# Kernel tuning notes

Hardware: AMD Instinct MI355X
Metric: run time of the kernel (lower is better)

Reference implementation:

```python
import jax, jax.numpy as jnp
import numpy as np

B, S, HID = 2, 2048, 2048
NH, NKV, HD = 8, 1, 256
GROUPS = NH // NKV
THETA = 10000.0


def _rope_cos_sin(position_ids, dtype):
    # inv_freq: [HD/2]
    inv_freq = 1.0 / (THETA ** (jnp.arange(0, HD, 2, dtype=jnp.float32) / HD))
    # freqs: [B, S, HD/2]
    freqs = position_ids.astype(jnp.float32)[:, :, None] * inv_freq[None, None, :]
    emb = jnp.concatenate([freqs, freqs], axis=-1)  # [B, S, HD]
    return emb.astype(dtype), None  # placeholder (cos/sin computed below)


def _rotate_half(x):
    x1, x2 = jnp.split(x, 2, axis=-1)
    return jnp.concatenate([-x2, x1], axis=-1)


def setup_inputs() -> dict:
    key = jax.random.key(0)
    ks = jax.random.split(key, 6)
    hidden_states = jax.random.normal(ks[0], (B, S, HID), dtype=jnp.float32)
    # causal additive mask, broadcast over heads: [B, 1, S, S]
    causal = jnp.tril(jnp.ones((S, S), dtype=bool))
    attention_mask = jnp.where(causal, 0.0, -1e9).astype(jnp.float32)[None, None] * jnp.ones((B, 1, 1, 1), jnp.float32)
    position_ids = jnp.broadcast_to(jnp.arange(S, dtype=jnp.int64 if jax.config.jax_enable_x64 else jnp.int32), (B, S))
    sc = 1.0 / np.sqrt(HID)
    Wq = jax.random.normal(ks[1], (HID, NH * HD), dtype=jnp.float32) * sc
    Wk = jax.random.normal(ks[2], (HID, NKV * HD), dtype=jnp.float32) * sc
    Wv = jax.random.normal(ks[3], (HID, NKV * HD), dtype=jnp.float32) * sc
    Wo = jax.random.normal(ks[4], (NH * HD, HID), dtype=jnp.float32) * sc
    return {"hidden_states": hidden_states, "attention_mask": attention_mask,
            "position_ids": position_ids, "Wq": Wq, "Wk": Wk, "Wv": Wv, "Wo": Wo}


def reference(hidden_states, attention_mask, position_ids, Wq, Wk, Wv, Wo):
    b, s, _ = hidden_states.shape
    # projections -> [b, h, s, d]
    q = (hidden_states @ Wq).reshape(b, s, NH, HD).transpose(0, 2, 1, 3)
    k = (hidden_states @ Wk).reshape(b, s, NKV, HD).transpose(0, 2, 1, 3)
    v = (hidden_states @ Wv).reshape(b, s, NKV, HD).transpose(0, 2, 1, 3)

    # RoPE cos/sin: [b, s, HD]
    inv_freq = 1.0 / (THETA ** (jnp.arange(0, HD, 2, dtype=jnp.float32) / HD))
    freqs = position_ids.astype(jnp.float32)[:, :, None] * inv_freq[None, None, :]
    emb = jnp.concatenate([freqs, freqs], axis=-1)
    cos = jnp.cos(emb).astype(hidden_states.dtype)[:, None]  # [b,1,s,HD]
    sin = jnp.sin(emb).astype(hidden_states.dtype)[:, None]
    q = q * cos + _rotate_half(q) * sin
    k = k * cos + _rotate_half(k) * sin

    # GQA without materializing repeated KV: q -> [b, g, rep, s, d]
    qg = q.reshape(b, NKV, GROUPS, s, HD)
    scale = 1.0 / np.sqrt(HD)
    scores = jnp.einsum('bgrqd,bgkd->bgrqk', qg, k) * scale  # [b,g,rep,s,s]
    scores = scores + attention_mask.reshape(b, 1, 1, s, s) if attention_mask.shape[1] == 1 else scores + attention_mask.reshape(b, NKV, GROUPS, s, s)
    attn = jax.nn.softmax(scores.astype(jnp.float32), axis=-1).astype(q.dtype)
    out = jnp.einsum('bgrqk,bgkd->bgrqd', attn, v)  # [b,g,rep,s,d]
    out = out.reshape(b, NH, s, HD).transpose(0, 2, 1, 3).reshape(b, s, NH * HD)
    attn_output = out @ Wo  # [b, s, HID]
    attn_weights = attn.reshape(b, NH, s, s)
    return attn_output, attn_weights
```

## Files before the change

### kernel.cpp

```cpp
#include <hip/hip_runtime.h>
#include <hip/hip_bf16.h>
#include <cstdint>


#define BB 2
#define SS 2048
#define HIDD 2048
#define NHH 8
#define HDD 256
#define L2E 1.44269504088896340736f
#define QSCALE 0.0625f

typedef float f32x4 __attribute__((ext_vector_type(4)));
typedef short short8 __attribute__((ext_vector_type(8)));
typedef __bf16 bf16x8 __attribute__((ext_vector_type(8)));
typedef __attribute__((address_space(1))) void gvoid;
typedef __attribute__((address_space(3))) void svoid;

__device__ __forceinline__ ushort f2bf(float f){
  union { float f; uint32_t u; } v; v.f = f;
  uint32_t r = (v.u + 0x7fffu + ((v.u >> 16) & 1u)) >> 16;
  return (ushort)r;
}
__device__ __forceinline__ float bf2f(ushort u){
  union { uint32_t u; float f; } v; v.u = ((uint32_t)u) << 16;
  return v.f;
}
__device__ __forceinline__ void gld_lds16(const ushort* gp, ushort* lp){
  __builtin_amdgcn_global_load_lds((gvoid*)gp, (svoid*)lp, 16, 0, 0);
}
__device__ __forceinline__ f32x4 mfma16(short8 a, short8 b, f32x4 c){
  return __builtin_amdgcn_mfma_f32_16x16x32_bf16(
      __builtin_bit_cast(bf16x8, a), __builtin_bit_cast(bf16x8, b), c, 0, 0, 0);
}

__global__ void k_convH(const float* __restrict__ Hf, ushort* __restrict__ Hb){
  const int n4 = (BB*SS*HIDD) >> 2;
  for (int i = blockIdx.x*256 + threadIdx.x; i < n4; i += gridDim.x*256){
    float4 v = ((const float4*)Hf)[i];
    ushort4 o; o.x=f2bf(v.x); o.y=f2bf(v.y); o.z=f2bf(v.z); o.w=f2bf(v.w);
    ((ushort4*)Hb)[i] = o;
  }
}

__global__ __launch_bounds__(256) void k_transW(const float* __restrict__ W,
                                                ushort* __restrict__ Wt,
                                                int N, int rowOff){
  __shared__ float t[64][65];
  const int n0 = blockIdx.x * 64, k0 = blockIdx.y * 64;
  const int tid = threadIdx.x;
  const int r = tid >> 4, c4 = (tid & 15) << 2;
  #pragma unroll
  for (int i = 0; i < 4; ++i){
    int rr = r + i*16;
    float4 v = *(const float4*)&W[(size_t)(k0 + rr) * N + n0 + c4];
    t[rr][c4] = v.x; t[rr][c4+1] = v.y; t[rr][c4+2] = v.z; t[rr][c4+3] = v.w;
  }
  __syncthreads();
  #pragma unroll
  for (int i = 0; i < 4; ++i){
    int nn = r + i*16;
    ushort4 o;
    o.x = f2bf(t[c4  ][nn]); o.y = f2bf(t[c4+1][nn]);
    o.z = f2bf(t[c4+2][nn]); o.w = f2bf(t[c4+3][nn]);
    *(ushort4*)&Wt[(size_t)(rowOff + n0 + nn) * 2048 + k0 + c4] = o;
  }
}

__global__ void k_costab(const int* __restrict__ pos, float2* __restrict__ cs){
  int i = blockIdx.x*256 + threadIdx.x;
  int d = i & 127, bs = i >> 7;
  float p = (float)pos[bs];
  float inv = exp2f(-(float)(2*d) * (13.287712379549449f / 256.0f));
  float f = p * inv;
  cs[i] = make_float2(cosf(f), sinf(f));
}

__global__ void k_rope(ushort* __restrict__ Qr, ushort* __restrict__ Kr,
                       const float2* __restrict__ cs){
  const int NQ = BB*SS*NHH*128;
  int i = blockIdx.x*256 + threadIdx.x;
  if (i < NQ){
    int d = i & 127, h = (i >> 7) & 7, bs = i >> 10;
    ushort* p = Qr + (size_t)bs*2048 + h*256 + d;
    float2 c = cs[bs*128 + d];
    float x1 = bf2f(p[0]), x2 = bf2f(p[128]);
    p[0]   = f2bf((x1*c.x - x2*c.y) * QSCALE);
    p[128] = f2bf((x2*c.x + x1*c.y) * QSCALE);
  } else if (i < NQ + BB*SS*128){
    int j = i - NQ;
    int d = j & 127, bs = j >> 7;
    ushort* p = Kr + (size_t)bs*256 + d;
    float2 c = cs[bs*128 + d];
    float x1 = bf2f(p[0]), x2 = bf2f(p[128]);
    p[0]   = f2bf(x1*c.x - x2*c.y);
    p[128] = f2bf(x2*c.x + x1*c.y);
  }
}

__global__ __launch_bounds__(256) void k_gemm(const ushort* __restrict__ A,
                                              const ushort* __restrict__ Bt,
                                              int Ksteps, int mode,
                                              float* __restrict__ Cf,
                                              ushort* __restrict__ Qr,
                                              ushort* __restrict__ Kr,
                                              ushort* __restrict__ Vt){
  __shared__ __align__(16) ushort As[128*32];
  __shared__ __align__(16) ushort Bs[128*32];
  const int tid = threadIdx.x;
  const int l = tid & 63, w = tid >> 6;
  const int lr = l & 15, lg = l >> 4;
  const int wr = (w >> 1) * 64, wc = (w & 1) * 64;
  const int m0 = blockIdx.y * 128, n0 = blockIdx.x * 128;
  f32x4 acc[4][4] = {};
  for (int kt = 0; kt < Ksteps; ++kt){
    const int kb = kt * 32;
    #pragma unroll
    for (int t = 0; t < 2; ++t){
      int r = t*64 + (tid >> 2), g = tid & 3;
      int gl = g ^ ((r >> 1) & 3);
      gld_lds16(A  + (size_t)(m0 + r) * 2048 + kb + gl*8, As + (t*256 + (tid & ~63))*8);
      gld_lds16(Bt + (size_t)(n0 + r) * 2048 + kb + gl*8, Bs + (t*256 + (tid & ~63))*8);
    }
    __syncthreads();
    short8 af[4], bf[4];
    #pragma unroll
    for (int mi = 0; mi < 4; ++mi){
      int r = wr + mi*16 + lr;
      af[mi] = *(const short8*)&As[r*32 + ((lg ^ ((r>>1)&3)) << 3)];
    }
    #pragma unroll
    for (int ni = 0; ni < 4; ++ni){
      int r = wc + ni*16 + lr;
      bf[ni] = *(const short8*)&Bs[r*32 + ((lg ^ ((r>>1)&3)) << 3)];
    }
    #pragma unroll
    for (int mi = 0; mi < 4; ++mi)
      #pragma unroll
      for (int ni = 0; ni < 4; ++ni)
        acc[mi][ni] = mfma16(af[mi], bf[ni], acc[mi][ni]);
    __syncthreads();
  }
  #pragma unroll
  for (int mi = 0; mi < 4; ++mi){
    #pragma unroll
    for (int ni = 0; ni < 4; ++ni){
      #pragma unroll
      for (int r = 0; r < 4; ++r){
        int row = m0 + wr + mi*16 + lg*4 + r;
        int nn  = n0 + wc + ni*16 + lr;
        float v = acc[mi][ni][r];
        if (mode == 0){
          Cf[(size_t)row * 2048 + nn] = v;
        } else {
          if (nn < 2048)      Qr[(size_t)row*2048 + nn] = f2bf(v);
          else if (nn < 2304) Kr[(size_t)row*256 + (nn - 2048)] = f2bf(v);
          else { int d = nn - 2304;
                 Vt[((size_t)(row >> 11) * 256 + d) * 2048 + (row & 2047)] = f2bf(v); }
        }
      }
    }
  }
}

__global__ __launch_bounds__(256) void k_stats(const ushort* __restrict__ Qr,
                                               const ushort* __restrict__ Kr,
                                               float* __restrict__ mpart,
                                               float* __restrict__ lpart){
  __shared__ __align__(16) ushort Ks[32*256];
  const int qt = blockIdx.x, ksp = blockIdx.y, bh = blockIdx.z;
  const int b = bh >> 3, h = bh & 7;
  const int q0 = qt * 64;
  const int nkt = (q0 + 64) >> 5;
  const int per = (nkt + 3) >> 2;
  const int t0 = ksp * per;
  const int t1 = min(nkt, t0 + per);
  const int tid = threadIdx.x;
  const int l = tid & 63, w = tid >> 6;
  const int lr = l & 15, lg = l >> 4;
  short8 qf[8];
  const ushort* qbase = Qr + ((size_t)(b*SS) + q0 + w*16 + lr) * 2048 + h*256;
  #pragma unroll
  for (int dc = 0; dc < 8; ++dc) qf[dc] = *(const short8*)&qbase[dc*32 + lg*8];
  float mrun[4], lrun[4];
  #pragma unroll
  for (int r = 0; r < 4; ++r){ mrun[r] = -3e38f; lrun[r] = 0.f; }
  for (int kt = t0; kt < t1; ++kt){
    const int k0 = kt * 32;
    #pragma unroll
    for (int t = 0; t < 4; ++t){
      int idx = t*256 + tid;
      int r = idx >> 5, g = idx & 31;
      int gl = g ^ (r & 7);
      gld_lds16(Kr + ((size_t)(b*SS) + k0 + r) * 256 + gl*8, Ks + (t*256 + (tid & ~63))*8);
    }
    __syncthreads();
    f32x4 sc0 = {0.f,0.f,0.f,0.f}, sc1 = {0.f,0.f,0.f,0.f};
    const int kr0 = lr, kr1 = 16 + lr;
    #pragma unroll
    for (int dc = 0; dc < 8; ++dc){
      short8 b0 = *(const short8*)&Ks[kr0*256 + ((dc*32 + lg*8) ^ ((kr0 & 7) << 3))];
      sc0 = mfma16(qf[dc], b0, sc0);
    }
    #pragma unroll
    for (int dc = 0; dc < 8; ++dc){
      short8 b1 = *(const short8*)&Ks[kr1*256 + ((dc*32 + lg*8) ^ ((kr1 & 7) << 3))];
      sc1 = mfma16(qf[dc], b1, sc1);
    }
    __syncthreads();
    #pragma unroll
    for (int r = 0; r < 4; ++r){
      const int qq = q0 + w*16 + lg*4 + r;
      float s0 = (k0 + lr       <= qq) ? sc0[r] : -3e38f;
      float s1 = (k0 + 16 + lr  <= qq) ? sc1[r] : -3e38f;
      float mx = fmaxf(s0, s1);
      #pragma unroll
      for (int d = 1; d < 16; d <<= 1) mx = fmaxf(mx, __shfl_xor(mx, d, 64));
      float mnew = fmaxf(mrun[r], mx);
      if (mnew > -1e37f){
        float ps = exp2f((s0 - mnew) * L2E) + exp2f((s1 - mnew) * L2E);
        #pragma unroll
        for (int d = 1; d < 16; d <<= 1) ps += __shfl_xor(ps, d, 64);
        lrun[r] = lrun[r] * exp2f((mrun[r] - mnew) * L2E) + ps;
        mrun[r] = mnew;
      }
    }
  }
  if (lr == 0){
    #pragma unroll
    for (int r = 0; r < 4; ++r){
      int qq = q0 + w*16 + lg*4 + r;
      size_t sidx = (size_t)ksp * (BB*NHH*SS) + (size_t)bh * SS + qq;
      mpart[sidx] = mrun[r];
      lpart[sidx] = lrun[r];
    }
  }
}

__global__ void k_merge(const float* __restrict__ mpart, const float* __restrict__ lpart,
                        float* __restrict__ mfin, float* __restrict__ invl){
  const int N = BB*NHH*SS;
  int i = blockIdx.x * 256 + threadIdx.x;
  if (i >= N) return;
  float m = -3e38f;
  #pragma unroll
  for (int s = 0; s < 4; ++s) m = fmaxf(m, mpart[s*N + i]);
  float lsum = 0.f;
  #pragma unroll
  for (int s = 0; s < 4; ++s){
    float ls = lpart[s*N + i];
    lsum += (ls > 0.f) ? ls * exp2f((mpart[s*N + i] - m) * L2E) : 0.f;
  }
  mfin[i] = m;
  invl[i] = 1.0f / lsum;
}

__global__ __launch_bounds__(256) void k_attn2(const ushort* __restrict__ Qr,
                                               const ushort* __restrict__ Kr,
                                               const ushort* __restrict__ Vt,
                                               const float* __restrict__ mfin,
                                               const float* __restrict__ invl,
                                               float* __restrict__ Wout,
                                               ushort* __restrict__ Ows){
  __shared__ __align__(16) ushort Ks[32*256];
  __shared__ __align__(16) ushort Vs[256*32];
  __shared__ __align__(16) ushort Ps[4][16*32];
  const int qt = (int)gridDim.x - 1 - (int)blockIdx.x;
  const int bh = blockIdx.y;
  const int b = bh >> 3, h = bh & 7;
  const int q0 = qt * 64;
  const int tid = threadIdx.x;
  const int l = tid & 63, w = tid >> 6;
  const int lr = l & 15, lg = l >> 4;
  short8 qf[8];
  const ushort* qbase = Qr + ((size_t)(b*SS) + q0 + w*16 + lr) * 2048 + h*256;
  #pragma unroll
  for (int dc = 0; dc < 8; ++dc) qf[dc] = *(const short8*)&qbase[dc*32 + lg*8];
  float mrow[4], il[4];
  #pragma unroll
  for (int r = 0; r < 4; ++r){
    int qq = q0 + w*16 + lg*4 + r;
    mrow[r] = mfin[bh*SS + qq];
    il[r]   = invl[bh*SS + qq];
  }
  f32x4 oacc[16] = {};
  const int nkt = (q0 + 64) >> 5;
  for (int kt = 0; kt < nkt; ++kt){
    const int k0 = kt * 32;
    #pragma unroll
    for (int t = 0; t < 4; ++t){
      int idx = t*256 + tid;
      int r = idx >> 5, g = idx & 31;
      int gl = g ^ (r & 7);
      gld_lds16(Kr + ((size_t)(b*SS) + k0 + r) * 256 + gl*8, Ks + (t*256 + (tid & ~63))*8);
    }
    #pragma unroll
    for (int t = 0; t < 4; ++t){
      int idx = t*256 + tid;
      int r = idx >> 2, g = idx & 3;
      int gl = g ^ ((r >> 1) & 3);
      gld_lds16(Vt + ((size_t)b*256 + r) * 2048 + k0 + gl*8, Vs + (t*256 + (tid & ~63))*8);
    }
    __syncthreads();
    f32x4 sc0 = {0.f,0.f,0.f,0.f}, sc1 = {0.f,0.f,0.f,0.f};
    const int kr0 = lr, kr1 = 16 + lr;
    #pragma unroll
    for (int dc = 0; dc < 8; ++dc){
      short8 b0 = *(const short8*)&Ks[kr0*256 + ((dc*32 + lg*8) ^ ((kr0 & 7) << 3))];
      sc0 = mfma16(qf[dc], b0, sc0);
    }
    #pragma unroll
    for (int dc = 0; dc < 8; ++dc){
      short8 b1 = *(const short8*)&Ks[kr1*256 + ((dc*32 + lg*8) ^ ((kr1 & 7) << 3))];
      sc1 = mfma16(qf[dc], b1, sc1);
    }
    #pragma unroll
    for (int r = 0; r < 4; ++r){
      const int qq = q0 + w*16 + lg*4 + r;
      const int kk0 = k0 + lr, kk1 = k0 + 16 + lr;
      float p0 = (kk0 <= qq) ? exp2f((sc0[r] - mrow[r]) * L2E) : 0.f;
      float p1 = (kk1 <= qq) ? exp2f((sc1[r] - mrow[r]) * L2E) : 0.f;
      float* wrp = Wout + ((size_t)bh * SS + qq) * SS;
      wrp[kk0] = p0 * il[r];
      wrp[kk1] = p1 * il[r];
      int row = lg*4 + r;
      int sw = ((row >> 1) & 3) << 3;
      Ps[w][row*32 + (lr ^ sw)]        = f2bf(p0);
      Ps[w][row*32 + ((16 + lr) ^ sw)] = f2bf(p1);
    }
    short8 pa = *(const short8*)&Ps[w][lr*32 + ((lg*8) ^ (((lr >> 1) & 3) << 3))];
    #pragma unroll
    for (int nf = 0; nf < 16; ++nf){
      int dr = nf*16 + lr;
      short8 vb = *(const short8*)&Vs[dr*32 + ((lg*8) ^ (((dr >> 1) & 3) << 3))];
      oacc[nf] = mfma16(pa, vb, oacc[nf]);
    }
    __syncthreads();
  }
  const int zc0 = q0 + 64;
  if (zc0 < SS){
    const int quads = (SS - zc0) >> 2;
    const float4 z4 = make_float4(0.f, 0.f, 0.f, 0.f);
    for (int rr = w; rr < 64; rr += 4){
      float* rowp = Wout + ((size_t)bh*SS + q0 + rr)*SS + zc0;
      for (int c = l; c < quads; c += 64)
        *(float4*)&rowp[c*4] = z4;
    }
  }
  #pragma unroll
  for (int nf = 0; nf < 16; ++nf){
    #pragma unroll
    for (int r = 0; r < 4; ++r){
      int qq = q0 + w*16 + lg*4 + r;
      int d  = nf*16 + lr;
      Ows[((size_t)(b*SS) + qq)*2048 + h*256 + d] = f2bf(oacc[nf][r] * il[r]);
    }
  }
}

extern "C" void kernel_launch(void* const* d_in, const int* in_sizes, int n_in,
                              void* d_out, int out_size, void* d_ws, size_t ws_size,
                              hipStream_t stream){
  const float* H  = (const float*)d_in[0];
  const int*  pos = (const int*)d_in[2];
  const float* Wq = (const float*)d_in[3];
  const float* Wk = (const float*)d_in[4];
  const float* Wv = (const float*)d_in[5];
  const float* Wo = (const float*)d_in[6];
  float* out = (float*)d_out;
  float* Wts = out + (size_t)BB*SS*HIDD;

  ushort* Hb = (ushort*)Wts;
  ushort* Wt = Hb + (size_t)BB*SS*HIDD;

  char* ws = (char*)d_ws;
  size_t off = 0;
  auto alloc = [&](size_t bytes)->char*{
    char* p = ws + off; off += (bytes + 255) & ~(size_t)255; return p;
  };
  ushort* Wot   = (ushort*)alloc((size_t)2048*2048*2);
  ushort* Qr    = (ushort*)alloc((size_t)BB*SS*NHH*HDD*2);
  ushort* Kr    = (ushort*)alloc((size_t)BB*SS*HDD*2);
  ushort* Vt    = (ushort*)alloc((size_t)BB*HDD*SS*2);
  float2* cst   = (float2*)alloc((size_t)BB*SS*128*8);
  float*  mpart = (float*)alloc((size_t)4*BB*NHH*SS*4);
  float*  lpart = (float*)alloc((size_t)4*BB*NHH*SS*4);
  float*  mfin  = (float*)alloc((size_t)BB*NHH*SS*4);
  float*  invl  = (float*)alloc((size_t)BB*NHH*SS*4);
  ushort* Ows   = (ushort*)alloc((size_t)BB*SS*NHH*HDD*2);
  (void)ws_size; (void)in_sizes; (void)n_in; (void)out_size;

  k_convH<<<2048, 256, 0, stream>>>(H, Hb);
  k_transW<<<dim3(32,32), 256, 0, stream>>>(Wq, Wt, 2048, 0);
  k_transW<<<dim3(4,32),  256, 0, stream>>>(Wk, Wt, 256, 2048);
  k_transW<<<dim3(4,32),  256, 0, stream>>>(Wv, Wt, 256, 2304);
  k_transW<<<dim3(32,32), 256, 0, stream>>>(Wo, Wot, 2048, 0);
  k_costab<<<(BB*SS*128)/256, 256, 0, stream>>>(pos, cst);
  k_gemm<<<dim3(20,32), 256, 0, stream>>>(Hb, Wt, 64, 1, nullptr, Qr, Kr, Vt);
  k_rope<<<(BB*SS*NHH*128 + BB*SS*128)/256, 256, 0, stream>>>(Qr, Kr, cst);
  k_stats<<<dim3(32,4,16), 256, 0, stream>>>(Qr, Kr, mpart, lpart);
  k_merge<<<(BB*NHH*SS)/256, 256, 0, stream>>>(mpart, lpart, mfin, invl);
  k_attn2<<<dim3(32,16), 256, 0, stream>>>(Qr, Kr, Vt, mfin, invl, Wts, Ows);
  k_gemm<<<dim3(16,32), 256, 0, stream>>>(Ows, Wot, 64, 0, out, nullptr, nullptr, nullptr);
}
```

Before: 724.0 us.

## Double attention key tile to 64, fuse prep kernels, and transpose V separately

Result: no change. 711.6 us (-1.7%).

```diff
diff --git a/kernel.cpp b/kernel.cpp
--- a/kernel.cpp
+++ b/kernel.cpp
@@ -34,20 +34,40 @@
       __builtin_bit_cast(bf16x8, a), __builtin_bit_cast(bf16x8, b), c, 0, 0, 0);
 }
 
-__global__ void k_convH(const float* __restrict__ Hf, ushort* __restrict__ Hb){
+__global__ void k_prep(const float* __restrict__ Hf, ushort* __restrict__ Hb,
+                       const int* __restrict__ pos, float2* __restrict__ cs){
   const int n4 = (BB*SS*HIDD) >> 2;
-  for (int i = blockIdx.x*256 + threadIdx.x; i < n4; i += gridDim.x*256){
-    float4 v = ((const float4*)Hf)[i];
-    ushort4 o; o.x=f2bf(v.x); o.y=f2bf(v.y); o.z=f2bf(v.z); o.w=f2bf(v.w);
-    ((ushort4*)Hb)[i] = o;
-  }
-}
-
-__global__ __launch_bounds__(256) void k_transW(const float* __restrict__ W,
-                                                ushort* __restrict__ Wt,
-                                                int N, int rowOff){
+  const int ncs = BB*SS*128;
+  for (int i = blockIdx.x*256 + threadIdx.x; i < n4 + ncs; i += gridDim.x*256){
+    if (i < n4){
+      float4 v = ((const float4*)Hf)[i];
+      ushort4 o; o.x=f2bf(v.x); o.y=f2bf(v.y); o.z=f2bf(v.z); o.w=f2bf(v.w);
+      ((ushort4*)Hb)[i] = o;
+    } else {
+      int j = i - n4;
+      int d = j & 127, bs = j >> 7;
+      float p = (float)pos[bs];
+      float inv = exp2f(-(float)(2*d) * (13.287712379549449f / 256.0f));
+      float f = p * inv;
+      cs[j] = make_float2(cosf(f), sinf(f));
+    }
+  }
+}
+
+__global__ __launch_bounds__(256) void k_transAll(const float* __restrict__ Wq,
+                                                  const float* __restrict__ Wk,
+                                                  const float* __restrict__ Wv,
+                                                  const float* __restrict__ Wo,
+                                                  ushort* __restrict__ Wt,
+                                                  ushort* __restrict__ Wot){
   __shared__ float t[64][65];
-  const int n0 = blockIdx.x * 64, k0 = blockIdx.y * 64;
+  const int z = blockIdx.x;
+  const float* W; ushort* dst; int N, rowOff, loc, nbx;
+  if (z < 1024){ W=Wq; dst=Wt;  N=2048; rowOff=0;    loc=z;      nbx=32; }
+  else if (z < 1152){ W=Wk; dst=Wt; N=256; rowOff=2048; loc=z-1024; nbx=4; }
+  else if (z < 1280){ W=Wv; dst=Wt; N=256; rowOff=2304; loc=z-1152; nbx=4; }
+  else { W=Wo; dst=Wot; N=2048; rowOff=0; loc=z-1280; nbx=32; }
+  const int n0 = (loc % nbx) * 64, k0 = (loc / nbx) * 64;
   const int tid = threadIdx.x;
   const int r = tid >> 4, c4 = (tid & 15) << 2;
   #pragma unroll
@@ -63,17 +83,8 @@
     ushort4 o;
     o.x = f2bf(t[c4  ][nn]); o.y = f2bf(t[c4+1][nn]);
     o.z = f2bf(t[c4+2][nn]); o.w = f2bf(t[c4+3][nn]);
-    *(ushort4*)&Wt[(size_t)(rowOff + n0 + nn) * 2048 + k0 + c4] = o;
-  }
-}
-
-__global__ void k_costab(const int* __restrict__ pos, float2* __restrict__ cs){
-  int i = blockIdx.x*256 + threadIdx.x;
-  int d = i & 127, bs = i >> 7;
-  float p = (float)pos[bs];
-  float inv = exp2f(-(float)(2*d) * (13.287712379549449f / 256.0f));
-  float f = p * inv;
-  cs[i] = make_float2(cosf(f), sinf(f));
+    *(ushort4*)&dst[(size_t)(rowOff + n0 + nn) * 2048 + k0 + c4] = o;
+  }
 }
 
 __global__ void k_rope(ushort* __restrict__ Qr, ushort* __restrict__ Kr,
@@ -104,7 +115,7 @@
                                               float* __restrict__ Cf,
                                               ushort* __restrict__ Qr,
                                               ushort* __restrict__ Kr,
-                                              ushort* __restrict__ Vt){
+                                              ushort* __restrict__ Vr){
   __shared__ __align__(16) ushort As[128*32];
   __shared__ __align__(16) ushort Bs[128*32];
   const int tid = threadIdx.x;
@@ -155,11 +166,37 @@
         } else {
           if (nn < 2048)      Qr[(size_t)row*2048 + nn] = f2bf(v);
           else if (nn < 2304) Kr[(size_t)row*256 + (nn - 2048)] = f2bf(v);
-          else { int d = nn - 2304;
-                 Vt[((size_t)(row >> 11) * 256 + d) * 2048 + (row & 2047)] = f2bf(v); }
+          else                Vr[(size_t)row*256 + (nn - 2304)] = f2bf(v);
         }
       }
     }
+  }
+}
+
+__global__ __launch_bounds__(256) void k_transV(const ushort* __restrict__ Vr,
+                                                ushort* __restrict__ Vt){
+  __shared__ ushort T[64][72];
+  const int bidx = blockIdx.x;
+  const int b = bidx >> 7, rest = bidx & 127;
+  const int s0 = (rest >> 2) * 64, d0 = (rest & 3) * 64;
+  const int tid = threadIdx.x;
+  #pragma unroll
+  for (int i = 0; i < 2; ++i){
+    int idx = i*256 + tid;
+    int r = idx >> 3, c = (idx & 7) * 8;
+    short8 v = *(const short8*)&Vr[((size_t)(b*SS) + s0 + r)*256 + d0 + c];
+    #pragma unroll
+    for (int j = 0; j < 8; ++j) T[r][c + j] = (ushort)v[j];
+  }
+  __syncthreads();
+  #pragma unroll
+  for (int i = 0; i < 2; ++i){
+    int idx = i*256 + tid;
+    int dr = idx >> 3, c = (idx & 7) * 8;
+    short8 o;
+    #pragma unroll
+    for (int j = 0; j < 8; ++j) o[j] = (short)T[c + j][dr];
+    *(short8*)&Vt[((size_t)(b*256) + d0 + dr)*2048 + s0 + c] = o;
   }
 }
 
@@ -167,11 +204,11 @@
                                                const ushort* __restrict__ Kr,
                                                float* __restrict__ mpart,
                                                float* __restrict__ lpart){
-  __shared__ __align__(16) ushort Ks[32*256];
+  __shared__ __align__(16) ushort Ks[64*256];
   const int qt = blockIdx.x, ksp = blockIdx.y, bh = blockIdx.z;
   const int b = bh >> 3, h = bh & 7;
   const int q0 = qt * 64;
-  const int nkt = (q0 + 64) >> 5;
+  const int nkt = (q0 + 64) >> 6;
   const int per = (nkt + 3) >> 2;
   const int t0 = ksp * per;
   const int t1 = min(nkt, t0 + per);
@@ -186,39 +223,40 @@
   #pragma unroll
   for (int r = 0; r < 4; ++r){ mrun[r] = -3e38f; lrun[r] = 0.f; }
   for (int kt = t0; kt < t1; ++kt){
-    const int k0 = kt * 32;
-    #pragma unroll
-    for (int t = 0; t < 4; ++t){
+    const int k0 = kt * 64;
+    #pragma unroll
+    for (int t = 0; t < 8; ++t){
       int idx = t*256 + tid;
       int r = idx >> 5, g = idx & 31;
       int gl = g ^ (r & 7);
       gld_lds16(Kr + ((size_t)(b*SS) + k0 + r) * 256 + gl*8, Ks + (t*256 + (tid & ~63))*8);
     }
     __syncthreads();
-    f32x4 sc0 = {0.f,0.f,0.f,0.f}, sc1 = {0.f,0.f,0.f,0.f};
-    const int kr0 = lr, kr1 = 16 + lr;
-    #pragma unroll
-    for (int dc = 0; dc < 8; ++dc){
-      short8 b0 = *(const short8*)&Ks[kr0*256 + ((dc*32 + lg*8) ^ ((kr0 & 7) << 3))];
-      sc0 = mfma16(qf[dc], b0, sc0);
-    }
-    #pragma unroll
-    for (int dc = 0; dc < 8; ++dc){
-      short8 b1 = *(const short8*)&Ks[kr1*256 + ((dc*32 + lg*8) ^ ((kr1 & 7) << 3))];
-      sc1 = mfma16(qf[dc], b1, sc1);
+    f32x4 sc[4] = {};
+    #pragma unroll
+    for (int j = 0; j < 4; ++j){
+      const int krj = j*16 + lr;
+      #pragma unroll
+      for (int dc = 0; dc < 8; ++dc){
+        short8 b8 = *(const short8*)&Ks[krj*256 + ((dc*32 + lg*8) ^ ((krj & 7) << 3))];
+        sc[j] = mfma16(qf[dc], b8, sc[j]);
+      }
     }
     __syncthreads();
     #pragma unroll
     for (int r = 0; r < 4; ++r){
       const int qq = q0 + w*16 + lg*4 + r;
-      float s0 = (k0 + lr       <= qq) ? sc0[r] : -3e38f;
-      float s1 = (k0 + 16 + lr  <= qq) ? sc1[r] : -3e38f;
-      float mx = fmaxf(s0, s1);
+      float s0 = (k0 + lr      <= qq) ? sc[0][r] : -3e38f;
+      float s1 = (k0 + 16 + lr <= qq) ? sc[1][r] : -3e38f;
+      float s2 = (k0 + 32 + lr <= qq) ? sc[2][r] : -3e38f;
+      float s3 = (k0 + 48 + lr <= qq) ? sc[3][r] : -3e38f;
+      float mx = fmaxf(fmaxf(s0, s1), fmaxf(s2, s3));
       #pragma unroll
       for (int d = 1; d < 16; d <<= 1) mx = fmaxf(mx, __shfl_xor(mx, d, 64));
       float mnew = fmaxf(mrun[r], mx);
       if (mnew > -1e37f){
-        float ps = exp2f((s0 - mnew) * L2E) + exp2f((s1 - mnew) * L2E);
+        float ps = exp2f((s0 - mnew) * L2E) + exp2f((s1 - mnew) * L2E)
+                 + exp2f((s2 - mnew) * L2E) + exp2f((s3 - mnew) * L2E);
         #pragma unroll
         for (int d = 1; d < 16; d <<= 1) ps += __shfl_xor(ps, d, 64);
         lrun[r] = lrun[r] * exp2f((mrun[r] - mnew) * L2E) + ps;
@@ -262,9 +300,9 @@
                                                const float* __restrict__ invl,
                                                float* __restrict__ Wout,
                                                ushort* __restrict__ Ows){
-  __shared__ __align__(16) ushort Ks[32*256];
-  __shared__ __align__(16) ushort Vs[256*32];
-  __shared__ __align__(16) ushort Ps[4][16*32];
+  __shared__ __align__(16) ushort Ks[64*256];
+  __shared__ __align__(16) ushort Vs[256*64];
+  __shared__ __align__(16) ushort Ps[4][16*64];
   const int qt = (int)gridDim.x - 1 - (int)blockIdx.x;
   const int bh = blockIdx.y;
   const int b = bh >> 3, h = bh & 7;
@@ -284,56 +322,57 @@
     il[r]   = invl[bh*SS + qq];
   }
   f32x4 oacc[16] = {};
-  const int nkt = (q0 + 64) >> 5;
+  const int nkt = (q0 + 64) >> 6;
   for (int kt = 0; kt < nkt; ++kt){
-    const int k0 = kt * 32;
-    #pragma unroll
-    for (int t = 0; t < 4; ++t){
+    const int k0 = kt * 64;
+    #pragma unroll
+    for (int t = 0; t < 8; ++t){
       int idx = t*256 + tid;
       int r = idx >> 5, g = idx & 31;
       int gl = g ^ (r & 7);
       gld_lds16(Kr + ((size_t)(b*SS) + k0 + r) * 256 + gl*8, Ks + (t*256 + (tid & ~63))*8);
     }
     #pragma unroll
-    for (int t = 0; t < 4; ++t){
+    for (int t = 0; t < 8; ++t){
       int idx = t*256 + tid;
-      int r = idx >> 2, g = idx & 3;
-      int gl = g ^ ((r >> 1) & 3);
+      int r = idx >> 3, g = idx & 7;
+      int gl = g ^ (r & 7);
       gld_lds16(Vt + ((size_t)b*256 + r) * 2048 + k0 + gl*8, Vs + (t*256 + (tid & ~63))*8);
     }
     __syncthreads();
-    f32x4 sc0 = {0.f,0.f,0.f,0.f}, sc1 = {0.f,0.f,0.f,0.f};
-    const int kr0 = lr, kr1 = 16 + lr;
-    #pragma unroll
-    for (int dc = 0; dc < 8; ++dc){
-      short8 b0 = *(const short8*)&Ks[kr0*256 + ((dc*32 + lg*8) ^ ((kr0 & 7) << 3))];
-      sc0 = mfma16(qf[dc], b0, sc0);
-    }
-    #pragma unroll
-    for (int dc = 0; dc < 8; ++dc){
-      short8 b1 = *(const short8*)&Ks[kr1*256 + ((dc*32 + lg*8) ^ ((kr1 & 7) << 3))];
-      sc1 = mfma16(qf[dc], b1, sc1);
+    f32x4 sc[4] = {};
+    #pragma unroll
+    for (int j = 0; j < 4; ++j){
+      const int krj = j*16 + lr;
+      #pragma unroll
+      for (int dc = 0; dc < 8; ++dc){
+        short8 b8 = *(const short8*)&Ks[krj*256 + ((dc*32 + lg*8) ^ ((krj & 7) << 3))];
+        sc[j] = mfma16(qf[dc], b8, sc[j]);
+      }
     }
     #pragma unroll
     for (int r = 0; r < 4; ++r){
       const int qq = q0 + w*16 + lg*4 + r;
-      const int kk0 = k0 + lr, kk1 = k0 + 16 + lr;
-      float p0 = (kk0 <= qq) ? exp2f((sc0[r] - mrow[r]) * L2E) : 0.f;
-      float p1 = (kk1 <= qq) ? exp2f((sc1[r] - mrow[r]) * L2E) : 0.f;
+      const int row = lg*4 + r;
       float* wrp = Wout + ((size_t)bh * SS + qq) * SS;
-      wrp[kk0] = p0 * il[r];
-      wrp[kk1] = p1 * il[r];
-      int row = lg*4 + r;
-      int sw = ((row >> 1) & 3) << 3;
-      Ps[w][row*32 + (lr ^ sw)]        = f2bf(p0);
-      Ps[w][row*32 + ((16 + lr) ^ sw)] = f2bf(p1);
-    }
-    short8 pa = *(const short8*)&Ps[w][lr*32 + ((lg*8) ^ (((lr >> 1) & 3) << 3))];
-    #pragma unroll
-    for (int nf = 0; nf < 16; ++nf){
-      int dr = nf*16 + lr;
-      short8 vb = *(const short8*)&Vs[dr*32 + ((lg*8) ^ (((dr >> 1) & 3) << 3))];
-      oacc[nf] = mfma16(pa, vb, oacc[nf]);
+      #pragma unroll
+      for (int j = 0; j < 4; ++j){
+        const int kk = k0 + j*16 + lr;
+        float p = (kk <= qq) ? exp2f((sc[j][r] - mrow[r]) * L2E) : 0.f;
+        wrp[kk] = p * il[r];
+        int chunk = j*2 + (lr >> 3);
+        Ps[w][row*64 + ((chunk ^ (row & 7)) << 3) + (lr & 7)] = f2bf(p);
+      }
+    }
+    #pragma unroll
+    for (int kc = 0; kc < 2; ++kc){
+      short8 pa = *(const short8*)&Ps[w][lr*64 + (((kc*4 + lg) ^ (lr & 7)) << 3)];
+      #pragma unroll
+      for (int nf = 0; nf < 16; ++nf){
+        int dr = nf*16 + lr;
+        short8 vb = *(const short8*)&Vs[dr*64 + (((kc*4 + lg) ^ (dr & 7)) << 3)];
+        oacc[nf] = mfma16(pa, vb, oacc[nf]);
+      }
     }
     __syncthreads();
   }
@@ -381,6 +420,7 @@
   ushort* Wot   = (ushort*)alloc((size_t)2048*2048*2);
   ushort* Qr    = (ushort*)alloc((size_t)BB*SS*NHH*HDD*2);
   ushort* Kr    = (ushort*)alloc((size_t)BB*SS*HDD*2);
+  ushort* Vr    = (ushort*)alloc((size_t)BB*SS*HDD*2);
   ushort* Vt    = (ushort*)alloc((size_t)BB*HDD*SS*2);
   float2* cst   = (float2*)alloc((size_t)BB*SS*128*8);
   float*  mpart = (float*)alloc((size_t)4*BB*NHH*SS*4);
@@ -390,13 +430,10 @@
   ushort* Ows   = (ushort*)alloc((size_t)BB*SS*NHH*HDD*2);
   (void)ws_size; (void)in_sizes; (void)n_in; (void)out_size;
 
-  k_convH<<<2048, 256, 0, stream>>>(H, Hb);
-  k_transW<<<dim3(32,32), 256, 0, stream>>>(Wq, Wt, 2048, 0);
-  k_transW<<<dim3(4,32),  256, 0, stream>>>(Wk, Wt, 256, 2048);
-  k_transW<<<dim3(4,32),  256, 0, stream>>>(Wv, Wt, 256, 2304);
-  k_transW<<<dim3(32,32), 256, 0, stream>>>(Wo, Wot, 2048, 0);
-  k_costab<<<(BB*SS*128)/256, 256, 0, stream>>>(pos, cst);
-  k_gemm<<<dim3(20,32), 256, 0, stream>>>(Hb, Wt, 64, 1, nullptr, Qr, Kr, Vt);
+  k_prep<<<2048, 256, 0, stream>>>(H, Hb, pos, cst);
+  k_transAll<<<2304, 256, 0, stream>>>(Wq, Wk, Wv, Wo, Wt, Wot);
+  k_gemm<<<dim3(20,32), 256, 0, stream>>>(Hb, Wt, 64, 1, nullptr, Qr, Kr, Vr);
+  k_transV<<<256, 256, 0, stream>>>(Vr, Vt);
   k_rope<<<(BB*SS*NHH*128 + BB*SS*128)/256, 256, 0, stream>>>(Qr, Kr, cst);
   k_stats<<<dim3(32,4,16), 256, 0, stream>>>(Qr, Kr, mpart, lpart);
   k_merge<<<(BB*NHH*SS)/256, 256, 0, stream>>>(mpart, lpart, mfin, invl);
```
